# Performance work log

Measured on AMD Instinct MI355X. Metric: run time of the kernel, lower is better.

The kernel has to match this reference:

```python
import jax, jax.numpy as jnp
import numpy as np

NFRAMES, BS, LATENT = 196, 128, 1024
E = 16            # number of object types (experts)
NJOINTS = 128     # max joints -> padded width
NFEATS = 6
INPUT_FEATS = NJOINTS * NFEATS  # 768


def setup_inputs() -> dict:
    key = jax.random.key(0)
    k1, k2, k3, k4 = jax.random.split(key, 4)
    output = jax.random.normal(k1, (NFRAMES, BS, LATENT), dtype=jnp.float32)
    object_types = jax.random.randint(k2, (BS,), 0, E)
    # stacked per-type Linear params, zero-padded to INPUT_FEATS
    W = jax.random.normal(k3, (E, LATENT, INPUT_FEATS), dtype=jnp.float32) * (1.0 / np.sqrt(LATENT))
    b = jax.random.normal(k4, (E, INPUT_FEATS), dtype=jnp.float32) * 0.01
    # valid joints per type in [8, NJOINTS]
    joint_counts = jax.random.randint(jax.random.fold_in(key, 7), (E,), 8, NJOINTS + 1)
    return {"output": output, "object_types": object_types, "W": W, "b": b,
            "joint_counts": joint_counts}


def reference(output, object_types, W, b, joint_counts):
    # per-expert valid output width and column mask [E, INPUT_FEATS]
    feat_counts = joint_counts * NFEATS
    col_mask = (jnp.arange(INPUT_FEATS)[None, :] < feat_counts[:, None]).astype(output.dtype)
    # gather per-sample expert params: Wg [BS, LATENT, F], bg/mg [BS, F]
    Wg = W[object_types]
    bg = b[object_types]
    mg = col_mask[object_types]
    # y[t,b,f] = sum_d output[t,b,d] * Wg[b,d,f] + bg[b,f], zero-padded past valid width
    y = (jnp.einsum('tbd,bdf->tbf', output, Wg) + bg[None]) * mg[None]
    y = y.reshape(NFRAMES, BS, NJOINTS, NFEATS)
    return jnp.transpose(y, (1, 2, 3, 0))  # (bs, njoints, nfeats, nframes)
```

## Files before the change

### kernel.cpp

```cpp
#include <hip/hip_runtime.h>
#include <hip/hip_bf16.h>


#define NFRAMES 196
#define TPAD    208
#define BSZ     128
#define DLAT    1024
#define FIN     768
#define BM      128
#define BK      32
#define KSTEPS  (DLAT / BK)
#define MTILES  (FIN / BM)
#define NBLK    (MTILES * BSZ)
#define NTHREADS 256

typedef short bf16x8 __attribute__((ext_vector_type(8)));
typedef float f32x4  __attribute__((ext_vector_type(4)));
typedef unsigned int u32x2 __attribute__((ext_vector_type(2)));
typedef unsigned int u32x4 __attribute__((ext_vector_type(4)));

__device__ __forceinline__ unsigned int pkbf(float lo, float hi) {
    unsigned short a = (unsigned short)__builtin_bit_cast(short, __float2bfloat16(lo));
    unsigned short b = (unsigned short)__builtin_bit_cast(short, __float2bfloat16(hi));
    return (unsigned int)a | ((unsigned int)b << 16);
}

#define BAR() do { asm volatile("s_waitcnt lgkmcnt(0)" ::: "memory"); \
                   __builtin_amdgcn_s_barrier(); } while (0)

template<int NF>
__device__ __forceinline__ void mfma_all(const short* __restrict__ Bp, const int* idxB,
                                         const bf16x8 (&af)[4], f32x4 (&acc)[4][7]) {
    #pragma unroll
    for (int nf = 0; nf < NF; ++nf) {
        bf16x8 bv = *reinterpret_cast<const bf16x8*>(&Bp[idxB[nf]]);
        #pragma unroll
        for (int f = 0; f < 4; ++f)
            acc[f][nf] = __builtin_amdgcn_mfma_f32_16x16x32_bf16(af[f], bv, acc[f][nf], 0, 0, 0);
    }
}

template<int NF>
__device__ __forceinline__ void epilogue(const f32x4 (&acc)[4][7], float* __restrict__ outB,
                                         const float* __restrict__ biasE, int fcb, int m0,
                                         int wr, int wc, int g, int lr) {
    #pragma unroll
    for (int f = 0; f < 4; ++f) {
        #pragma unroll
        for (int rr = 0; rr < 4; ++rr) {
            const int fcol = m0 + wr * 64 + f * 16 + g * 4 + rr;
            const float bb = biasE[fcol];
            const bool  val = fcol < fcb;
            #pragma unroll
            for (int nf = 0; nf < NF; ++nf) {
                const int t = wc * 112 + nf * 16 + lr;
                if (t < NFRAMES)
                    outB[fcol * NFRAMES + t] = val ? (acc[f][nf][rr] + bb) : 0.f;
            }
        }
    }
}

__global__ __launch_bounds__(NTHREADS, 2)
void fused_expert_gemm(const float* __restrict__ X,
                       const int*   __restrict__ otypes,
                       const float* __restrict__ W,
                       const float* __restrict__ Bias,
                       const int*   __restrict__ jc,
                       float*       __restrict__ out)
{
    __shared__ short As[BM * BK];
    __shared__ short Bs[TPAD * BK];

    const int hw = blockIdx.x;
    const int mt = hw >> 7;
    const int b  = hw & 127;
    const int m0 = mt * BM;

    const int tid = threadIdx.x;
    const int e   = otypes[b];
    const int fcb = jc[e] * 6;
    float* outB = out + (size_t)b * (FIN * NFRAMES);

    if (m0 >= fcb) {
        f32x4 zz = {0.f, 0.f, 0.f, 0.f};
        f32x4* dst = reinterpret_cast<f32x4*>(outB + m0 * NFRAMES);
        const int total = (BM * NFRAMES) / 4;
        for (int i = tid; i < total; i += NTHREADS) dst[i] = zz;
        return;
    }

    const int wave = tid >> 6;
    const int lane = tid & 63;
    const int lr   = lane & 15;
    const int g    = lane >> 4;
    const int wr   = wave >> 1;
    const int wc   = wave & 1;

    const int mb  = tid & 31;
    const int kb  = tid >> 5;
    const int kbe = (kb + (mb >> 2)) & 7;
    const int ko = tid & 3;
    const int rw = tid >> 2;

    const f32x4* __restrict__ Xv = reinterpret_cast<const f32x4*>(X);
    const f32x4* __restrict__ Wv = reinterpret_cast<const f32x4*>(W);
    const f32x4 fz = {0.f, 0.f, 0.f, 0.f};

    f32x4 wa[4];
    f32x4 xb[4][2];

    int idxA[4], idxB[7];
    #pragma unroll
    for (int f = 0; f < 4; ++f)
        idxA[f] = (wr * 64 + f * 16 + lr) * BK + g * 8;
    #pragma unroll
    for (int nf = 0; nf < 7; ++nf)
        idxB[nf] = (wc * 112 + nf * 16 + lr) * BK + g * 8;

    f32x4 acc[4][7];
    #pragma unroll
    for (int f = 0; f < 4; ++f)
        #pragma unroll
        for (int nf = 0; nf < 7; ++nf) acc[f][nf] = fz;

    auto load_stage = [&](int kk) {
        #pragma unroll
        for (int i = 0; i < 4; ++i)
            wa[i] = Wv[(e * DLAT + kk + kbe * 4 + i) * (FIN / 4) + (m0 >> 2) + mb];
        #pragma unroll
        for (int p = 0; p < 4; ++p) {
            const int n = p * 64 + rw;
            if (n < NFRAMES) {
                const int base = (n * BSZ + b) * (DLAT / 4) + (kk >> 2) + ko * 2;
                xb[p][0] = Xv[base];
                xb[p][1] = Xv[base + 1];
            } else { xb[p][0] = fz; xb[p][1] = fz; }
        }
    };

    auto write_stage = [&]() {
        #pragma unroll
        for (int jj = 0; jj < 4; ++jj) {
            const int r = (mb + jj) & 3;
            u32x2 v = { pkbf(wa[0][r], wa[1][r]), pkbf(wa[2][r], wa[3][r]) };
            *reinterpret_cast<u32x2*>(&As[(mb * 4 + r) * BK + kbe * 4]) = v;
        }
        #pragma unroll
        for (int p = 0; p < 4; ++p) {
            const int n = p * 64 + rw;
            if (n < TPAD) {
                u32x4 v = { pkbf(xb[p][0][0], xb[p][0][1]), pkbf(xb[p][0][2], xb[p][0][3]),
                            pkbf(xb[p][1][0], xb[p][1][1]), pkbf(xb[p][1][2], xb[p][1][3]) };
                *reinterpret_cast<u32x4*>(&Bs[n * BK + ko * 8]) = v;
            }
        }
    };

    load_stage(0);

    #pragma unroll 1
    for (int ks = 0; ks < KSTEPS; ++ks) {
        BAR();
        write_stage();
        if (ks + 1 < KSTEPS)
            load_stage((ks + 1) * BK);
        BAR();

        bf16x8 af[4];
        #pragma unroll
        for (int f = 0; f < 4; ++f)
            af[f] = *reinterpret_cast<const bf16x8*>(&As[idxA[f]]);
        if (wc == 0) mfma_all<7>(Bs, idxB, af, acc);
        else         mfma_all<6>(Bs, idxB, af, acc);
    }

    const float* biasE = Bias + e * FIN;
    if (wc == 0) epilogue<7>(acc, outB, biasE, fcb, m0, wr, wc, g, lr);
    else         epilogue<6>(acc, outB, biasE, fcb, m0, wr, wc, g, lr);
}

extern "C" void kernel_launch(void* const* d_in, const int* in_sizes, int n_in,
                              void* d_out, int out_size, void* d_ws, size_t ws_size,
                              hipStream_t stream) {
    const float* X    = (const float*)d_in[0];
    const int*   ot   = (const int*)d_in[1];
    const float* W    = (const float*)d_in[2];
    const float* Bias = (const float*)d_in[3];
    const int*   jc   = (const int*)d_in[4];
    float*       out  = (float*)d_out;

    dim3 grid(NBLK);
    dim3 block(NTHREADS);
    hipLaunchKernelGGL(fused_expert_gemm, grid, block, 0, stream,
                       X, ot, W, Bias, jc, out);
}
```

Measured before the change: 107.9 us.

## Split frame dimension across two blocks and raise occupancy target

Each (batch, M-tile) block is split into two blocks covering frames 0-111 and 112-195, doubling the grid and shrinking the per-thread accumulator from 4x7 to 4x4 tiles. Launch bounds move from 2 to 3 waves per SIMD, and block indices are remapped with an 8-way interleave. The aim is more parallelism and better latency hiding, at the cost of loading and converting the W tile twice.

```diff
diff --git a/kernel.cpp b/kernel.cpp
--- a/kernel.cpp
+++ b/kernel.cpp
@@ -1,9 +1,9 @@
 #include <hip/hip_runtime.h>
 #include <hip/hip_bf16.h>
+#include <stdint.h>
 
 
 #define NFRAMES 196
-#define TPAD    208
 #define BSZ     128
 #define DLAT    1024
 #define FIN     768
@@ -11,8 +11,9 @@
 #define BK      32
 #define KSTEPS  (DLAT / BK)
 #define MTILES  (FIN / BM)
-#define NBLK    (MTILES * BSZ)
+#define NBLK    (2 * MTILES * BSZ)
 #define NTHREADS 256
+#define BROWS   112
 
 typedef short bf16x8 __attribute__((ext_vector_type(8)));
 typedef float f32x4  __attribute__((ext_vector_type(4)));
@@ -29,11 +30,17 @@
                    __builtin_amdgcn_s_barrier(); } while (0)
 
 template<int NF>
-__device__ __forceinline__ void mfma_all(const short* __restrict__ Bp, const int* idxB,
-                                         const bf16x8 (&af)[4], f32x4 (&acc)[4][7]) {
+__device__ __forceinline__ void compute_step(const short* __restrict__ Ab,
+                                             const short* __restrict__ Bb,
+                                             const int* idxA, const int* idxB,
+                                             f32x4 (&acc)[4][4]) {
+    bf16x8 af[4];
+    #pragma unroll
+    for (int f = 0; f < 4; ++f)
+        af[f] = *reinterpret_cast<const bf16x8*>(&Ab[idxA[f]]);
     #pragma unroll
     for (int nf = 0; nf < NF; ++nf) {
-        bf16x8 bv = *reinterpret_cast<const bf16x8*>(&Bp[idxB[nf]]);
+        bf16x8 bv = *reinterpret_cast<const bf16x8*>(&Bb[idxB[nf]]);
         #pragma unroll
         for (int f = 0; f < 4; ++f)
             acc[f][nf] = __builtin_amdgcn_mfma_f32_16x16x32_bf16(af[f], bv, acc[f][nf], 0, 0, 0);
@@ -41,9 +48,9 @@
 }
 
 template<int NF>
-__device__ __forceinline__ void epilogue(const f32x4 (&acc)[4][7], float* __restrict__ outB,
+__device__ __forceinline__ void epilogue(const f32x4 (&acc)[4][4], float* __restrict__ outB,
                                          const float* __restrict__ biasE, int fcb, int m0,
-                                         int wr, int wc, int g, int lr) {
+                                         int t0w, int wr, int g, int lr) {
     #pragma unroll
     for (int f = 0; f < 4; ++f) {
         #pragma unroll
@@ -53,7 +60,7 @@
             const bool  val = fcol < fcb;
             #pragma unroll
             for (int nf = 0; nf < NF; ++nf) {
-                const int t = wc * 112 + nf * 16 + lr;
+                const int t = t0w + nf * 16 + lr;
                 if (t < NFRAMES)
                     outB[fcol * NFRAMES + t] = val ? (acc[f][nf][rr] + bb) : 0.f;
             }
@@ -61,7 +68,18 @@
     }
 }
 
-__global__ __launch_bounds__(NTHREADS, 2)
+template<int NV4>
+__device__ __forceinline__ void fillz(float* __restrict__ base, int tid) {
+    const f32x4 zz = {0.f, 0.f, 0.f, 0.f};
+    const int total = BM * NV4;
+    for (int i = tid; i < total; i += NTHREADS) {
+        const int r = i / NV4;
+        const int c = i - r * NV4;
+        *reinterpret_cast<f32x4*>(base + r * NFRAMES + c * 4) = zz;
+    }
+}
+
+__global__ __launch_bounds__(NTHREADS, 3)
 void fused_expert_gemm(const float* __restrict__ X,
                        const int*   __restrict__ otypes,
                        const float* __restrict__ W,
@@ -70,23 +88,28 @@
                        float*       __restrict__ out)
 {
     __shared__ short As[BM * BK];
-    __shared__ short Bs[TPAD * BK];
-
-    const int hw = blockIdx.x;
-    const int mt = hw >> 7;
-    const int b  = hw & 127;
-    const int m0 = mt * BM;
+    __shared__ short Bs[BROWS * BK];
+
+    const int hw      = blockIdx.x;
+    const int logical = (hw & 7) * (NBLK / 8) + (hw >> 3);
+    const int nh      = logical & 1;
+    const int l2      = logical >> 1;
+    const int b       = l2 / MTILES;
+    const int mt      = l2 - b * MTILES;
+    const int m0      = mt * BM;
 
     const int tid = threadIdx.x;
     const int e   = otypes[b];
     const int fcb = jc[e] * 6;
     float* outB = out + (size_t)b * (FIN * NFRAMES);
 
+    const int t0   = nh * 112;
+    const int RMAX = nh ? 96 : 112;
+
     if (m0 >= fcb) {
-        f32x4 zz = {0.f, 0.f, 0.f, 0.f};
-        f32x4* dst = reinterpret_cast<f32x4*>(outB + m0 * NFRAMES);
-        const int total = (BM * NFRAMES) / 4;
-        for (int i = tid; i < total; i += NTHREADS) dst[i] = zz;
+        float* base = outB + (size_t)m0 * NFRAMES + t0;
+        if (nh == 0) fillz<28>(base, tid);
+        else         fillz<21>(base, tid);
         return;
     }
 
@@ -96,46 +119,58 @@
     const int g    = lane >> 4;
     const int wr   = wave >> 1;
     const int wc   = wave & 1;
+    const int r0   = wc * (nh ? 48 : 64);
+    const bool nf4 = (nh == 0) && (wc == 0);
+    const int t0w  = t0 + r0;
 
     const int mb  = tid & 31;
     const int kb  = tid >> 5;
     const int kbe = (kb + (mb >> 2)) & 7;
     const int ko = tid & 3;
     const int rw = tid >> 2;
+    const bool p1act = (64 + rw) < RMAX;
 
     const f32x4* __restrict__ Xv = reinterpret_cast<const f32x4*>(X);
     const f32x4* __restrict__ Wv = reinterpret_cast<const f32x4*>(W);
-    const f32x4 fz = {0.f, 0.f, 0.f, 0.f};
 
     f32x4 wa[4];
-    f32x4 xb[4][2];
-
-    int idxA[4], idxB[7];
+    f32x4 xb[2][2];
+
+    int trow[2];
+    {
+        int n0 = rw, n1 = 64 + rw;
+        int tg0 = t0 + n0, tg1 = t0 + n1;
+        trow[0] = tg0 < NFRAMES ? tg0 : NFRAMES - 1;
+        trow[1] = tg1 < NFRAMES ? tg1 : NFRAMES - 1;
+    }
+
+    int idxA[4], idxB[4];
     #pragma unroll
     for (int f = 0; f < 4; ++f)
         idxA[f] = (wr * 64 + f * 16 + lr) * BK + g * 8;
     #pragma unroll
-    for (int nf = 0; nf < 7; ++nf)
-        idxB[nf] = (wc * 112 + nf * 16 + lr) * BK + g * 8;
-
-    f32x4 acc[4][7];
+    for (int nf = 0; nf < 4; ++nf)
+        idxB[nf] = (r0 + nf * 16 + lr) * BK + g * 8;
+
+    f32x4 acc[4][4];
     #pragma unroll
     for (int f = 0; f < 4; ++f)
         #pragma unroll
-        for (int nf = 0; nf < 7; ++nf) acc[f][nf] = fz;
+        for (int nf = 0; nf < 4; ++nf) acc[f][nf] = {0.f, 0.f, 0.f, 0.f};
 
     auto load_stage = [&](int kk) {
         #pragma unroll
         for (int i = 0; i < 4; ++i)
             wa[i] = Wv[(e * DLAT + kk + kbe * 4 + i) * (FIN / 4) + (m0 >> 2) + mb];
-        #pragma unroll
-        for (int p = 0; p < 4; ++p) {
-            const int n = p * 64 + rw;
-            if (n < NFRAMES) {
-                const int base = (n * BSZ + b) * (DLAT / 4) + (kk >> 2) + ko * 2;
-                xb[p][0] = Xv[base];
-                xb[p][1] = Xv[base + 1];
-            } else { xb[p][0] = fz; xb[p][1] = fz; }
+        {
+            const int base0 = (trow[0] * BSZ + b) * (DLAT / 4) + (kk >> 2) + ko * 2;
+            xb[0][0] = Xv[base0];
+            xb[0][1] = Xv[base0 + 1];
+        }
+        if (p1act) {
+            const int base1 = (trow[1] * BSZ + b) * (DLAT / 4) + (kk >> 2) + ko * 2;
+            xb[1][0] = Xv[base1];
+            xb[1][1] = Xv[base1 + 1];
         }
     };
 
@@ -146,14 +181,15 @@
             u32x2 v = { pkbf(wa[0][r], wa[1][r]), pkbf(wa[2][r], wa[3][r]) };
             *reinterpret_cast<u32x2*>(&As[(mb * 4 + r) * BK + kbe * 4]) = v;
         }
-        #pragma unroll
-        for (int p = 0; p < 4; ++p) {
-            const int n = p * 64 + rw;
-            if (n < TPAD) {
-                u32x4 v = { pkbf(xb[p][0][0], xb[p][0][1]), pkbf(xb[p][0][2], xb[p][0][3]),
-                            pkbf(xb[p][1][0], xb[p][1][1]), pkbf(xb[p][1][2], xb[p][1][3]) };
-                *reinterpret_cast<u32x4*>(&Bs[n * BK + ko * 8]) = v;
-            }
+        {
+            u32x4 v = { pkbf(xb[0][0][0], xb[0][0][1]), pkbf(xb[0][0][2], xb[0][0][3]),
+                        pkbf(xb[0][1][0], xb[0][1][1]), pkbf(xb[0][1][2], xb[0][1][3]) };
+            *reinterpret_cast<u32x4*>(&Bs[rw * BK + ko * 8]) = v;
+        }
+        if (p1act) {
+            u32x4 v = { pkbf(xb[1][0][0], xb[1][0][1]), pkbf(xb[1][0][2], xb[1][0][3]),
+                        pkbf(xb[1][1][0], xb[1][1][1]), pkbf(xb[1][1][2], xb[1][1][3]) };
+            *reinterpret_cast<u32x4*>(&Bs[(64 + rw) * BK + ko * 8]) = v;
         }
     };
 
@@ -167,17 +203,13 @@
             load_stage((ks + 1) * BK);
         BAR();
 
-        bf16x8 af[4];
-        #pragma unroll
-        for (int f = 0; f < 4; ++f)
-            af[f] = *reinterpret_cast<const bf16x8*>(&As[idxA[f]]);
-        if (wc == 0) mfma_all<7>(Bs, idxB, af, acc);
-        else         mfma_all<6>(Bs, idxB, af, acc);
+        if (nf4) compute_step<4>(As, Bs, idxA, idxB, acc);
+        else     compute_step<3>(As, Bs, idxA, idxB, acc);
     }
 
     const float* biasE = Bias + e * FIN;
-    if (wc == 0) epilogue<7>(acc, outB, biasE, fcb, m0, wr, wc, g, lr);
-    else         epilogue<6>(acc, outB, biasE, fcb, m0, wr, wc, g, lr);
+    if (nf4) epilogue<4>(acc, outB, biasE, fcb, m0, t0w, wr, g, lr);
+    else     epilogue<3>(acc, outB, biasE, fcb, m0, t0w, wr, g, lr);
 }
 
 extern "C" void kernel_launch(void* const* d_in, const int* in_sizes, int n_in,
```

New measurement: 197.9 us. 83.4% more time.
